# Optimization experiments

Hardware: AMD Instinct MI355X
Metric: run time of the kernel (lower is better)

Reference implementation:

```python
import jax, jax.numpy as jnp
import numpy as np

KEY_DIM = 1024
SCALE = KEY_DIM ** -0.5


def setup_inputs() -> dict:
    key = jax.random.key(0)
    k1, k2, k3, k4 = jax.random.split(key, 4)
    B, S, E = 4, 2048, 1024
    x = jax.random.normal(k1, (B, S, E), dtype=jnp.float32)
    WQ = jax.random.normal(k2, (KEY_DIM, E), dtype=jnp.float32) * (E ** -0.5)
    WK = jax.random.normal(k3, (KEY_DIM, E), dtype=jnp.float32) * (E ** -0.5)
    WV = jax.random.normal(k4, (KEY_DIM, E), dtype=jnp.float32) * (E ** -0.5)
    return {"x": x, "WQ": WQ, "WK": WK, "WV": WV}


def reference(x, WQ, WK, WV):
    # x: [B, S, E]; Linear(bias=False) weights are [out, in] as in torch.
    q = jnp.einsum('bse,ke->bsk', x, WQ)   # [B, S, K]
    k = jnp.einsum('bse,ke->bsk', x, WK)   # [B, S, K]
    v = jnp.einsum('bse,ve->bsv', x, WV)   # [B, S, V]
    scores = jnp.einsum('bsk,btk->bst', q, k) * SCALE  # [B, S, S]
    # Faithful to torch: mask where tril(scores) == 0 (upper triangle).
    masked = jnp.where(jnp.tril(scores) == 0, -jnp.inf, scores)
    attn = jax.nn.softmax(masked, axis=-1)
    return jnp.einsum('bst,btv->bsv', attn, v)  # dropout=0.0 -> identity
```

## Files before the change

### kernel.cpp

```cpp
#include <hip/hip_runtime.h>

typedef _Float16 f16x8 __attribute__((ext_vector_type(8)));
typedef unsigned short u16x8v __attribute__((ext_vector_type(8)));
typedef unsigned short u16x4v __attribute__((ext_vector_type(4)));
typedef float f32x4 __attribute__((ext_vector_type(4)));

constexpr int SEQ = 2048;
constexpr int DIM = 1024;
constexpr int BATCH = 4;
constexpr size_t NBS = (size_t)BATCH * SEQ * DIM;

static __device__ __forceinline__ unsigned short f2h(float f) {
    return __builtin_bit_cast(unsigned short, (_Float16)f);
}
static __device__ __forceinline__ float h2f(unsigned short u) {
    return (float)__builtin_bit_cast(_Float16, u);
}
static __device__ __forceinline__ f16x8 ldsld(const unsigned short* p) {
    return __builtin_bit_cast(f16x8, *(const u16x8v*)p);
}
static __device__ __forceinline__ void gld_lds16(const unsigned short* g, unsigned short* l) {
    __builtin_amdgcn_global_load_lds(
        (const __attribute__((address_space(1))) void*)g,
        (__attribute__((address_space(3))) void*)l, 16, 0, 0);
}

__global__ __launch_bounds__(256) void cvt_all(
    const float* __restrict__ X,
    const float* __restrict__ W0, const float* __restrict__ W1,
    const float* __restrict__ W2,
    unsigned short* __restrict__ Xf, unsigned short* __restrict__ Wf,
    unsigned short* __restrict__ WqT, unsigned short* __restrict__ WkT)
{
    __shared__ __attribute__((aligned(16))) unsigned short T[64][72];
    const int b = blockIdx.x;
    const int t = threadIdx.x;
    if (b < 11264) {
        const float* src;
        unsigned short* dst;
        int i;
        if (b < 8192) {
            src = X; dst = Xf;
            i = b * 256 + t;
        } else {
            const int wb = b - 8192;
            const int z = wb >> 10;
            src = (z == 0) ? W0 : (z == 1) ? W1 : W2;
            dst = Wf + (size_t)z * DIM * DIM;
            i = (wb & 1023) * 256 + t;
        }
        float4 f = ((const float4*)src)[i];
        u16x4v h;
        h.x = f2h(f.x); h.y = f2h(f.y); h.z = f2h(f.z); h.w = f2h(f.w);
        ((u16x4v*)dst)[i] = h;
        return;
    }
    const int tb = b - 11264;
    const float* src = (tb < 256) ? W0 : W1;
    unsigned short* dst = (tb < 256) ? WqT : WkT;
    const int tile = tb & 255;
    const int tk = (tile >> 4) * 64;
    const int te = (tile & 15) * 64;
    const int cu = t & 15, kr4 = t >> 4;
#pragma unroll
    for (int p = 0; p < 4; ++p) {
        const int k = p * 16 + kr4;
        float4 v = *(const float4*)(src + (size_t)(tk + k) * DIM + te + cu * 4);
        T[cu * 4 + 0][k] = f2h(v.x);
        T[cu * 4 + 1][k] = f2h(v.y);
        T[cu * 4 + 2][k] = f2h(v.z);
        T[cu * 4 + 3][k] = f2h(v.w);
    }
    __syncthreads();
    const int un = t & 7, er = t >> 3;
#pragma unroll
    for (int p = 0; p < 2; ++p) {
        const int e = p * 32 + er;
        *(u16x8v*)(dst + (size_t)(te + e) * DIM + tk + un * 8) =
            *(const u16x8v*)&T[e][un * 8];
    }
}

__global__ __launch_bounds__(256) void mt_gemm(
    const unsigned short* __restrict__ WkTp, const unsigned short* __restrict__ WqTp,
    unsigned short* __restrict__ Mt)
{
    __shared__ __attribute__((aligned(16))) unsigned short Ah[128 * 64];
    __shared__ __attribute__((aligned(16))) unsigned short Bh[128 * 64];
    const int m0 = blockIdx.x * 128, n0 = blockIdx.y * 128;
    const int tid = threadIdx.x;
    const int w = tid >> 6, lane = tid & 63, q = lane >> 4, c = lane & 15;
    const int wrow = (w >> 1) * 64, wcol = (w & 1) * 64;
    const int g8 = lane >> 3;
    const int cu = (lane & 7) ^ g8;
    const int srow = w * 8 + g8;
    const int scol = cu * 8;
    unsigned short* lA = Ah + w * 512;
    unsigned short* lB = Bh + w * 512;
    const int c7 = c & 7;

    f32x4 acc[4][4];
#pragma unroll
    for (int a = 0; a < 4; ++a)
#pragma unroll
        for (int bq = 0; bq < 4; ++bq) acc[a][bq] = (f32x4){0.f, 0.f, 0.f, 0.f};

    for (int k0 = 0; k0 < DIM; k0 += 64) {
        __syncthreads();
        {
            const size_t ga = (size_t)(m0 + srow) * DIM + k0 + scol;
            const size_t gb = (size_t)(n0 + srow) * DIM + k0 + scol;
#pragma unroll
            for (int j = 0; j < 4; ++j) {
                gld_lds16(WkTp + ga + (size_t)(j * 32) * DIM, lA + j * 2048);
                gld_lds16(WqTp + gb + (size_t)(j * 32) * DIM, lB + j * 2048);
            }
        }
        __syncthreads();
#pragma unroll
        for (int kk = 0; kk < 2; ++kk) {
            f16x8 af[4], bf[4];
#pragma unroll
            for (int mi = 0; mi < 4; ++mi)
                af[mi] = ldsld(Ah + (wrow + mi * 16 + c) * 64 + (((kk << 2) + q) ^ c7) * 8);
#pragma unroll
            for (int ni = 0; ni < 4; ++ni)
                bf[ni] = ldsld(Bh + (wcol + ni * 16 + c) * 64 + (((kk << 2) + q) ^ c7) * 8);
#pragma unroll
            for (int mi = 0; mi < 4; ++mi)
#pragma unroll
                for (int ni = 0; ni < 4; ++ni)
                    acc[mi][ni] = __builtin_amdgcn_mfma_f32_16x16x32_f16(af[mi], bf[ni], acc[mi][ni], 0, 0, 0);
        }
    }
#pragma unroll
    for (int mi = 0; mi < 4; ++mi)
#pragma unroll
        for (int ni = 0; ni < 4; ++ni) {
            const int col = n0 + wcol + ni * 16 + c;
#pragma unroll
            for (int r = 0; r < 4; ++r) {
                const int row = m0 + wrow + mi * 16 + q * 4 + r;
                Mt[(size_t)row * DIM + col] = f2h(acc[mi][ni][r]);
            }
        }
}

__global__ __launch_bounds__(256) void yv_gemm(
    const unsigned short* __restrict__ Xf, const unsigned short* __restrict__ Mt,
    const unsigned short* __restrict__ Wvf,
    unsigned short* __restrict__ Yf, unsigned short* __restrict__ Vt)
{
    __shared__ __attribute__((aligned(16))) unsigned short Ah[128 * 64];
    __shared__ __attribute__((aligned(16))) unsigned short Bh[128 * 64];
    const int m0 = blockIdx.x * 128, n0 = blockIdx.y * 128, z = blockIdx.z;
    const unsigned short* Wz = z ? Wvf : Mt;
    const int tid = threadIdx.x;
    const int w = tid >> 6, lane = tid & 63, q = lane >> 4, c = lane & 15;
    const int wrow = (w >> 1) * 64, wcol = (w & 1) * 64;
    const int g8 = lane >> 3;
    const int cu = (lane & 7) ^ g8;
    const int srow = w * 8 + g8;
    const int scol = cu * 8;
    unsigned short* lA = Ah + w * 512;
    unsigned short* lB = Bh + w * 512;
    const int c7 = c & 7;

    f32x4 acc[4][4];
#pragma unroll
    for (int a = 0; a < 4; ++a)
#pragma unroll
        for (int b = 0; b < 4; ++b) acc[a][b] = (f32x4){0.f, 0.f, 0.f, 0.f};

    for (int k0 = 0; k0 < DIM; k0 += 64) {
        __syncthreads();
        {
            const size_t ga = (size_t)(m0 + srow) * DIM + k0 + scol;
            const size_t gb = (size_t)(n0 + srow) * DIM + k0 + scol;
#pragma unroll
            for (int j = 0; j < 4; ++j) {
                gld_lds16(Xf + ga + (size_t)(j * 32) * DIM, lA + j * 2048);
                gld_lds16(Wz + gb + (size_t)(j * 32) * DIM, lB + j * 2048);
            }
        }
        __syncthreads();
#pragma unroll
        for (int kk = 0; kk < 2; ++kk) {
            f16x8 ah[4], bh[4];
#pragma unroll
            for (int mi = 0; mi < 4; ++mi)
                ah[mi] = ldsld(Ah + (wrow + mi * 16 + c) * 64 + (((kk << 2) + q) ^ c7) * 8);
#pragma unroll
            for (int ni = 0; ni < 4; ++ni)
                bh[ni] = ldsld(Bh + (wcol + ni * 16 + c) * 64 + (((kk << 2) + q) ^ c7) * 8);
#pragma unroll
            for (int mi = 0; mi < 4; ++mi)
#pragma unroll
                for (int ni = 0; ni < 4; ++ni)
                    acc[mi][ni] = __builtin_amdgcn_mfma_f32_16x16x32_f16(ah[mi], bh[ni], acc[mi][ni], 0, 0, 0);
        }
    }

    if (z == 1) {
#pragma unroll
        for (int mi = 0; mi < 4; ++mi) {
            const int mg = m0 + wrow + mi * 16 + q * 4;
            const int bb = mg >> 11, ss = mg & (SEQ - 1);
#pragma unroll
            for (int ni = 0; ni < 4; ++ni) {
                const int col = n0 + wcol + ni * 16 + c;
                u16x4v v;
                v.x = f2h(acc[mi][ni][0]);
                v.y = f2h(acc[mi][ni][1]);
                v.z = f2h(acc[mi][ni][2]);
                v.w = f2h(acc[mi][ni][3]);
                *(u16x4v*)(Vt + ((size_t)bb * DIM + col) * SEQ + ss) = v;
            }
        }
    } else {
#pragma unroll
        for (int mi = 0; mi < 4; ++mi)
#pragma unroll
            for (int ni = 0; ni < 4; ++ni) {
                const int col = n0 + wcol + ni * 16 + c;
#pragma unroll
                for (int r = 0; r < 4; ++r) {
                    const int row = m0 + wrow + mi * 16 + q * 4 + r;
                    Yf[(size_t)row * DIM + col] = f2h(acc[mi][ni][r]);
                }
            }
    }
}

__global__ __launch_bounds__(256) void scores_gemm1b(
    const unsigned short* __restrict__ Q, const unsigned short* __restrict__ K,
    unsigned short* __restrict__ S)
{
    __shared__ __attribute__((aligned(16))) unsigned short Ah[128 * 64];
    __shared__ __attribute__((aligned(16))) unsigned short Bh[128 * 64];
    const int flat = blockIdx.x;
    const int wg = (flat & 7) * 68 + (flat >> 3);
    const int b = wg / 136;
    const int t = wg - b * 136;
    int ti = (int)((__builtin_sqrtf(8.f * t + 1.f) - 1.f) * 0.5f);
    while ((ti + 1) * (ti + 2) / 2 <= t) ++ti;
    while (ti * (ti + 1) / 2 > t) --ti;
    const int tj = t - ti * (ti + 1) / 2;
    const int i0 = ti * 128, j0 = tj * 128;
    const unsigned short* Qb = Q + (size_t)b * SEQ * DIM;
    const unsigned short* Kb = K + (size_t)b * SEQ * DIM;
    unsigned short* Sb = S + (size_t)b * SEQ * SEQ;
    const int tid = threadIdx.x;
    const int w = tid >> 6, lane = tid & 63, q = lane >> 4, c = lane & 15;
    const int wrow = (w >> 1) * 64, wcol = (w & 1) * 64;
    const int g8 = lane >> 3;
    const int cu = (lane & 7) ^ g8;
    const int srow = w * 8 + g8;
    const int scol = cu * 8;
    unsigned short* lA = Ah + w * 512;
    unsigned short* lB = Bh + w * 512;
    const int c7 = c & 7;

    f32x4 acc[4][4];
#pragma unroll
    for (int a = 0; a < 4; ++a)
#pragma unroll
        for (int bq = 0; bq < 4; ++bq) acc[a][bq] = (f32x4){0.f, 0.f, 0.f, 0.f};

    for (int k0 = 0; k0 < DIM; k0 += 64) {
        __syncthreads();
        {
            const size_t ga = (size_t)(i0 + srow) * DIM + k0 + scol;
            const size_t gb = (size_t)(j0 + srow) * DIM + k0 + scol;
#pragma unroll
            for (int j = 0; j < 4; ++j) {
                gld_lds16(Qb + ga + (size_t)(j * 32) * DIM, lA + j * 2048);
                gld_lds16(Kb + gb + (size_t)(j * 32) * DIM, lB + j * 2048);
            }
        }
        __syncthreads();
#pragma unroll
        for (int kk = 0; kk < 2; ++kk) {
            f16x8 ah[4], bh[4];
#pragma unroll
            for (int mi = 0; mi < 4; ++mi)
                ah[mi] = ldsld(Ah + (wrow + mi * 16 + c) * 64 + (((kk << 2) + q) ^ c7) * 8);
#pragma unroll
            for (int ni = 0; ni < 4; ++ni)
                bh[ni] = ldsld(Bh + (wcol + ni * 16 + c) * 64 + (((kk << 2) + q) ^ c7) * 8);
#pragma unroll
            for (int mi = 0; mi < 4; ++mi)
#pragma unroll
                for (int ni = 0; ni < 4; ++ni)
                    acc[mi][ni] = __builtin_amdgcn_mfma_f32_16x16x32_f16(ah[mi], bh[ni], acc[mi][ni], 0, 0, 0);
        }
    }
#pragma unroll
    for (int mi = 0; mi < 4; ++mi)
#pragma unroll
        for (int ni = 0; ni < 4; ++ni) {
            const int col = j0 + wcol + ni * 16 + c;
#pragma unroll
            for (int r = 0; r < 4; ++r) {
                const int row = i0 + wrow + mi * 16 + q * 4 + r;
                const float sc = acc[mi][ni][r] * 0.03125f;
                Sb[(size_t)row * SEQ + col] =
                    (sc == 0.f) ? (unsigned short)0xFC00u : f2h(sc);
            }
        }
}

__global__ __launch_bounds__(256) void softmax_row_b(
    const unsigned short* __restrict__ S, unsigned short* __restrict__ P)
{
    const int i = blockIdx.x, t = threadIdx.x;
    const size_t ro = ((size_t)blockIdx.y * SEQ + i) * SEQ;
    const int wid = t >> 6, lane = t & 63;
    __shared__ float redm[4], reds[4];
    const int j0 = t * 8;
    const int rti = (i & ~127) + 128;
    float sv[8];
    float mx = -__builtin_inff();
    if (j0 <= i) {
        u16x8v raw = *(const u16x8v*)(S + ro + j0);
#pragma unroll
        for (int u = 0; u < 8; ++u) {
            float s = (j0 + u <= i) ? h2f(raw[u]) : -__builtin_inff();
            sv[u] = s;
            mx = fmaxf(mx, s);
        }
    } else {
#pragma unroll
        for (int u = 0; u < 8; ++u) sv[u] = -__builtin_inff();
    }
#pragma unroll
    for (int off = 1; off < 64; off <<= 1) mx = fmaxf(mx, __shfl_xor(mx, off));
    if (lane == 0) redm[wid] = mx;
    __syncthreads();
    const float M = fmaxf(fmaxf(redm[0], redm[1]), fmaxf(redm[2], redm[3]));
    float sum = 0.f;
#pragma unroll
    for (int u = 0; u < 8; ++u) {
        float e = __expf(sv[u] - M);
        sv[u] = e;
        sum += e;
    }
#pragma unroll
    for (int off = 1; off < 64; off <<= 1) sum += __shfl_xor(sum, off);
    if (lane == 0) reds[wid] = sum;
    __syncthreads();
    const float rinv = 1.f / (reds[0] + reds[1] + reds[2] + reds[3]);
    if (j0 < rti) {
        u16x8v o;
#pragma unroll
        for (int u = 0; u < 8; ++u) o[u] = f2h(sv[u] * rinv);
        *(u16x8v*)(P + ro + j0) = o;
    }
}

__global__ __launch_bounds__(256) void pv_gemm(
    const unsigned short* __restrict__ Pm, const unsigned short* __restrict__ Vt,
    float* __restrict__ Out)
{
    __shared__ __attribute__((aligned(16))) unsigned short Ps[128 * 64];
    __shared__ __attribute__((aligned(16))) unsigned short Vs[128 * 64];
    const int flat = blockIdx.x;
    const int wg = (flat & 7) * 64 + (flat >> 3);
    const int i0t = wg & 15;
    const int grp = wg >> 4;
    const int b = grp >> 3;
    const int d0 = (grp & 7) * 128;
    const int i0 = i0t * 128;
    const int tid = threadIdx.x;
    const int w = tid >> 6, lane = tid & 63, q = lane >> 4, c = lane & 15;
    const int wrow = (w >> 1) * 64, wcol = (w & 1) * 64;
    const int g8 = lane >> 3;
    const int cu = (lane & 7) ^ g8;
    const int srow = w * 8 + g8;
    const int scol = cu * 8;
    unsigned short* lA = Ps + w * 512;
    unsigned short* lB = Vs + w * 512;
    const int c7 = c & 7;

    f32x4 acc[4][4];
#pragma unroll
    for (int a = 0; a < 4; ++a)
#pragma unroll
        for (int bq = 0; bq < 4; ++bq) acc[a][bq] = (f32x4){0.f, 0.f, 0.f, 0.f};

    const int njs = 2 * i0t + 2;

    for (int ks = 0; ks < njs; ++ks) {
        const int j0 = ks * 64;
        __syncthreads();
        {
            const size_t gpa = ((size_t)b * SEQ + i0 + srow) * SEQ + j0 + scol;
            const size_t gva = ((size_t)b * DIM + d0 + srow) * SEQ + j0 + scol;
#pragma unroll
            for (int j = 0; j < 4; ++j) {
                gld_lds16(Pm + gpa + (size_t)(j * 32) * SEQ, lA + j * 2048);
                gld_lds16(Vt + gva + (size_t)(j * 32) * SEQ, lB + j * 2048);
            }
        }
        __syncthreads();
#pragma unroll
        for (int kk = 0; kk < 2; ++kk) {
            f16x8 ah[4], bh[4];
#pragma unroll
            for (int mi = 0; mi < 4; ++mi)
                ah[mi] = ldsld(Ps + (wrow + mi * 16 + c) * 64 + (((kk << 2) + q) ^ c7) * 8);
#pragma unroll
            for (int ni = 0; ni < 4; ++ni)
                bh[ni] = ldsld(Vs + (wcol + ni * 16 + c) * 64 + (((kk << 2) + q) ^ c7) * 8);
#pragma unroll
            for (int mi = 0; mi < 4; ++mi)
#pragma unroll
                for (int ni = 0; ni < 4; ++ni)
                    acc[mi][ni] = __builtin_amdgcn_mfma_f32_16x16x32_f16(ah[mi], bh[ni], acc[mi][ni], 0, 0, 0);
        }
    }
#pragma unroll
    for (int mi = 0; mi < 4; ++mi)
#pragma unroll
        for (int ni = 0; ni < 4; ++ni) {
            const int dcol = d0 + wcol + ni * 16 + c;
#pragma unroll
            for (int r = 0; r < 4; ++r) {
                const int i = i0 + wrow + mi * 16 + q * 4 + r;
                Out[((size_t)b * SEQ + i) * DIM + dcol] = acc[mi][ni][r];
            }
        }
}

extern "C" void kernel_launch(void* const* d_in, const int* in_sizes, int n_in,
                              void* d_out, int out_size, void* d_ws, size_t ws_size,
                              hipStream_t stream)
{
    (void)out_size; (void)ws_size;
    const float* X = nullptr;
    const float* Wv[3] = {nullptr, nullptr, nullptr};
    int nw = 0;
    for (int i = 0; i < n_in; ++i) {
        if (in_sizes[i] == (int)NBS)
            X = (const float*)d_in[i];
        else if (nw < 3)
            Wv[nw++] = (const float*)d_in[i];
    }

    unsigned short* ws = (unsigned short*)d_ws;
    unsigned short* Yf = ws;
    unsigned short* Vt = ws + 2 * NBS;
    unsigned short* Xf = ws + 3 * NBS;
    unsigned short* Pp = ws + 3 * NBS;
    unsigned short* Sb = ws + 5 * NBS;
    unsigned short* Wf = ws + 7 * NBS;
    unsigned short* Mtb = Wf + (size_t)3 * DIM * DIM;
    unsigned short* WqT = Mtb + (size_t)DIM * DIM;
    unsigned short* WkT = WqT + (size_t)DIM * DIM;
    float* Out = (float*)d_out;

    cvt_all<<<dim3(8192 + 3072 + 512), 256, 0, stream>>>(
        X, Wv[0], Wv[1], Wv[2], Xf, Wf, WqT, WkT);

    mt_gemm<<<dim3(8, 8), 256, 0, stream>>>(WkT, WqT, Mtb);

    yv_gemm<<<dim3(64, 8, 2), 256, 0, stream>>>(
        Xf, Mtb, Wf + (size_t)2 * DIM * DIM, Yf, Vt);

    scores_gemm1b<<<dim3(544), 256, 0, stream>>>(Yf, Xf, Sb);
    softmax_row_b<<<dim3(SEQ, BATCH), 256, 0, stream>>>(Sb, Pp);

    pv_gemm<<<dim3(512), 256, 0, stream>>>(Pp, Vt, Out);
}
```

Measured before the change: 241.0 us.

## Rewrite Y/V projection GEMM as 256x256 eight-wave double-buffered pipelined kernel

Replaces the 128x128, 4-wave Y/V GEMM with a 256x256 tile using 8 waves and 128KB of LDS split into two A/B buffers. Global-to-LDS loads for the next k-slices are interleaved with MFMA phases under explicit vmcnt waits, raw s_barrier and setprio, so memory traffic overlaps compute and each operand is reused across a larger tile. The trade-offs are only 256 blocks, one block per CU because of the LDS footprint, and more accumulator registers, which could limit occupancy or cause tail effects.

```diff
diff --git a/kernel.cpp b/kernel.cpp
--- a/kernel.cpp
+++ b/kernel.cpp
@@ -23,6 +23,9 @@
     __builtin_amdgcn_global_load_lds(
         (const __attribute__((address_space(1))) void*)g,
         (__attribute__((address_space(3))) void*)l, 16, 0, 0);
+}
+static __device__ __forceinline__ void barrier_mf() {
+    asm volatile("s_barrier" ::: "memory");
 }
 
 __global__ __launch_bounds__(256) void cvt_all(
@@ -146,87 +149,120 @@
         }
 }
 
-__global__ __launch_bounds__(256) void yv_gemm(
+__global__ __launch_bounds__(512) void yv8_gemm(
     const unsigned short* __restrict__ Xf, const unsigned short* __restrict__ Mt,
     const unsigned short* __restrict__ Wvf,
     unsigned short* __restrict__ Yf, unsigned short* __restrict__ Vt)
 {
-    __shared__ __attribute__((aligned(16))) unsigned short Ah[128 * 64];
-    __shared__ __attribute__((aligned(16))) unsigned short Bh[128 * 64];
-    const int m0 = blockIdx.x * 128, n0 = blockIdx.y * 128, z = blockIdx.z;
-    const unsigned short* Wz = z ? Wvf : Mt;
+    __shared__ __attribute__((aligned(16))) unsigned short L[65536];
+    unsigned short* A0 = L;
+    unsigned short* B0 = L + 16384;
+    unsigned short* A1 = L + 32768;
+    unsigned short* B1 = L + 49152;
+
+    const int m0 = blockIdx.x * 256, n0 = blockIdx.y * 256, z = blockIdx.z;
+    const unsigned short* Bg = z ? Wvf : Mt;
     const int tid = threadIdx.x;
-    const int w = tid >> 6, lane = tid & 63, q = lane >> 4, c = lane & 15;
-    const int wrow = (w >> 1) * 64, wcol = (w & 1) * 64;
-    const int g8 = lane >> 3;
-    const int cu = (lane & 7) ^ g8;
-    const int srow = w * 8 + g8;
-    const int scol = cu * 8;
-    unsigned short* lA = Ah + w * 512;
-    unsigned short* lB = Bh + w * 512;
-    const int c7 = c & 7;
-
-    f32x4 acc[4][4];
-#pragma unroll
-    for (int a = 0; a < 4; ++a)
-#pragma unroll
-        for (int b = 0; b < 4; ++b) acc[a][b] = (f32x4){0.f, 0.f, 0.f, 0.f};
-
-    for (int k0 = 0; k0 < DIM; k0 += 64) {
-        __syncthreads();
-        {
-            const size_t ga = (size_t)(m0 + srow) * DIM + k0 + scol;
-            const size_t gb = (size_t)(n0 + srow) * DIM + k0 + scol;
-#pragma unroll
-            for (int j = 0; j < 4; ++j) {
-                gld_lds16(Xf + ga + (size_t)(j * 32) * DIM, lA + j * 2048);
-                gld_lds16(Wz + gb + (size_t)(j * 32) * DIM, lB + j * 2048);
-            }
-        }
-        __syncthreads();
-#pragma unroll
-        for (int kk = 0; kk < 2; ++kk) {
-            f16x8 ah[4], bh[4];
-#pragma unroll
-            for (int mi = 0; mi < 4; ++mi)
-                ah[mi] = ldsld(Ah + (wrow + mi * 16 + c) * 64 + (((kk << 2) + q) ^ c7) * 8);
-#pragma unroll
-            for (int ni = 0; ni < 4; ++ni)
-                bh[ni] = ldsld(Bh + (wcol + ni * 16 + c) * 64 + (((kk << 2) + q) ^ c7) * 8);
-#pragma unroll
-            for (int mi = 0; mi < 4; ++mi)
-#pragma unroll
-                for (int ni = 0; ni < 4; ++ni)
-                    acc[mi][ni] = __builtin_amdgcn_mfma_f32_16x16x32_f16(ah[mi], bh[ni], acc[mi][ni], 0, 0, 0);
-        }
-    }
+    const int w = tid >> 6, lane = tid & 63;
+    const int wm = w >> 2, wn = w & 3;
+    const int c = lane & 15, q = lane >> 4, c7 = c & 7;
+    const int sl8 = lane >> 3;
+    const int gu = ((lane & 7) ^ sl8) * 8;
+
+    auto stage = [&](const unsigned short* G, int roff, int T, unsigned short* Lb, int h) {
+        const int rb0 = h * 128 + w * 16;
+        const int kb = T * 64 + gu;
+        gld_lds16(G + (size_t)(roff + rb0 + sl8) * DIM + kb, Lb + rb0 * 64 + lane * 8);
+        gld_lds16(G + (size_t)(roff + rb0 + 8 + sl8) * DIM + kb, Lb + (rb0 + 8) * 64 + lane * 8);
+    };
+    auto rdA = [&](const unsigned short* LA, int fr, int kk) {
+        const int row = wm * 128 + fr * 16 + c;
+        return ldsld(LA + row * 64 + (((kk << 2) + q) ^ c7) * 8);
+    };
+    auto rdB = [&](const unsigned short* LB, int fb, int kk) {
+        const int row = wn * 64 + fb * 16 + c;
+        return ldsld(LB + row * 64 + (((kk << 2) + q) ^ c7) * 8);
+    };
+
+    f32x4 acc[8][4];
+#pragma unroll
+    for (int a = 0; a < 8; ++a)
+#pragma unroll
+        for (int bq = 0; bq < 4; ++bq) acc[a][bq] = (f32x4){0.f, 0.f, 0.f, 0.f};
+    f16x8 bfr[4][2];
+
+#define PH(LAp, LBp, p, STAGES, LOADB)                                          \
+    {                                                                           \
+        if (LOADB) {                                                            \
+            _Pragma("unroll") for (int fb = 0; fb < 4; ++fb) {                  \
+                bfr[fb][0] = rdB(LBp, fb, 0);                                   \
+                bfr[fb][1] = rdB(LBp, fb, 1);                                   \
+            }                                                                   \
+        }                                                                       \
+        f16x8 a00 = rdA(LAp, 2 * (p), 0),     a01 = rdA(LAp, 2 * (p), 1);       \
+        f16x8 a10 = rdA(LAp, 2 * (p) + 1, 0), a11 = rdA(LAp, 2 * (p) + 1, 1);   \
+        STAGES;                                                                 \
+        barrier_mf();                                                           \
+        __builtin_amdgcn_s_setprio(1);                                          \
+        _Pragma("unroll") for (int fb = 0; fb < 4; ++fb) {                      \
+            acc[2*(p)][fb]   = __builtin_amdgcn_mfma_f32_16x16x32_f16(a00, bfr[fb][0], acc[2*(p)][fb],   0, 0, 0); \
+            acc[2*(p)][fb]   = __builtin_amdgcn_mfma_f32_16x16x32_f16(a01, bfr[fb][1], acc[2*(p)][fb],   0, 0, 0); \
+            acc[2*(p)+1][fb] = __builtin_amdgcn_mfma_f32_16x16x32_f16(a10, bfr[fb][0], acc[2*(p)+1][fb], 0, 0, 0); \
+            acc[2*(p)+1][fb] = __builtin_amdgcn_mfma_f32_16x16x32_f16(a11, bfr[fb][1], acc[2*(p)+1][fb], 0, 0, 0); \
+        }                                                                       \
+        __builtin_amdgcn_s_setprio(0);                                          \
+        barrier_mf();                                                           \
+    }
+
+    stage(Xf, m0, 0, A0, 0); stage(Xf, m0, 0, A0, 1);
+    stage(Bg, n0, 0, B0, 0); stage(Bg, n0, 0, B0, 1);
+    stage(Bg, n0, 1, B1, 0); stage(Bg, n0, 1, B1, 1);
+
+    for (int it = 0; it < 8; ++it) {
+        const int u = 2 * it;
+        const bool nt = it < 7;
+        asm volatile("s_waitcnt vmcnt(4)" ::: "memory");
+        barrier_mf();
+        PH(A0, B0, 0, { stage(Xf, m0, u + 1, A1, 0); }, true);
+        PH(A0, B0, 1, { stage(Xf, m0, u + 1, A1, 1); }, false);
+        PH(A0, B0, 2, { if (nt) stage(Bg, n0, u + 2, B0, 0); }, false);
+        PH(A0, B0, 3, { if (nt) stage(Bg, n0, u + 2, B0, 1); }, false);
+        if (nt) asm volatile("s_waitcnt vmcnt(4)" ::: "memory");
+        else    asm volatile("s_waitcnt vmcnt(0)" ::: "memory");
+        barrier_mf();
+        PH(A1, B1, 0, { if (nt) stage(Xf, m0, u + 2, A0, 0); }, true);
+        PH(A1, B1, 1, { if (nt) stage(Xf, m0, u + 2, A0, 1); }, false);
+        PH(A1, B1, 2, { if (nt) stage(Bg, n0, u + 3, B1, 0); }, false);
+        PH(A1, B1, 3, { if (nt) stage(Bg, n0, u + 3, B1, 1); }, false);
+    }
+#undef PH
 
     if (z == 1) {
 #pragma unroll
-        for (int mi = 0; mi < 4; ++mi) {
-            const int mg = m0 + wrow + mi * 16 + q * 4;
+        for (int fr = 0; fr < 8; ++fr) {
+            const int mg = m0 + wm * 128 + fr * 16 + q * 4;
             const int bb = mg >> 11, ss = mg & (SEQ - 1);
 #pragma unroll
-            for (int ni = 0; ni < 4; ++ni) {
-                const int col = n0 + wcol + ni * 16 + c;
+            for (int fb = 0; fb < 4; ++fb) {
+                const int col = n0 + wn * 64 + fb * 16 + c;
                 u16x4v v;
-                v.x = f2h(acc[mi][ni][0]);
-                v.y = f2h(acc[mi][ni][1]);
-                v.z = f2h(acc[mi][ni][2]);
-                v.w = f2h(acc[mi][ni][3]);
+                v.x = f2h(acc[fr][fb][0]);
+                v.y = f2h(acc[fr][fb][1]);
+                v.z = f2h(acc[fr][fb][2]);
+                v.w = f2h(acc[fr][fb][3]);
                 *(u16x4v*)(Vt + ((size_t)bb * DIM + col) * SEQ + ss) = v;
             }
         }
     } else {
 #pragma unroll
-        for (int mi = 0; mi < 4; ++mi)
-#pragma unroll
-            for (int ni = 0; ni < 4; ++ni) {
-                const int col = n0 + wcol + ni * 16 + c;
+        for (int fr = 0; fr < 8; ++fr)
+#pragma unroll
+            for (int fb = 0; fb < 4; ++fb) {
+                const int col = n0 + wn * 64 + fb * 16 + c;
 #pragma unroll
                 for (int r = 0; r < 4; ++r) {
-                    const int row = m0 + wrow + mi * 16 + q * 4 + r;
-                    Yf[(size_t)row * DIM + col] = f2h(acc[mi][ni][r]);
+                    const int row = m0 + wm * 128 + fr * 16 + q * 4 + r;
+                    Yf[(size_t)row * DIM + col] = f2h(acc[fr][fb][r]);
                 }
             }
     }
@@ -464,7 +500,7 @@
 
     mt_gemm<<<dim3(8, 8), 256, 0, stream>>>(WkT, WqT, Mtb);
 
-    yv_gemm<<<dim3(64, 8, 2), 256, 0, stream>>>(
+    yv8_gemm<<<dim3(32, 4, 2), 512, 0, stream>>>(
         Xf, Mtb, Wf + (size_t)2 * DIM * DIM, Yf, Vt);
 
     scores_gemm1b<<<dim3(544), 256, 0, stream>>>(Yf, Xf, Sb);
```

Measured after the change: 235.6 us. 2.2% less time.
